# Kernel optimization log

Hardware: AMD Instinct MI355X
Metric: run time of the kernel (lower is better)

The kernel has to match this reference:

```python
import jax, jax.numpy as jnp
import numpy as np

N = 100000
E = 600000
D = 128          # in_channels
D_OUT = 128      # out_channels


def setup_inputs() -> dict:
    key = jax.random.key(0)
    ks = jax.random.split(key, 8)
    node_embeddings = jax.random.normal(ks[0], (N, D), dtype=jnp.float32)
    edge_index = jax.random.randint(ks[1], (2, E), 0, N, dtype=jnp.int64)
    s = 1.0 / np.sqrt(D)
    W_src = jax.random.uniform(ks[2], (D, D), minval=-s, maxval=s, dtype=jnp.float32)
    W_tgt = jax.random.uniform(ks[3], (D, D), minval=-s, maxval=s, dtype=jnp.float32)
    s2 = 1.0 / np.sqrt(2 * D)
    W_proj = jax.random.uniform(ks[4], (2 * D, D_OUT), minval=-s2, maxval=s2, dtype=jnp.float32)
    b_proj = jax.random.uniform(ks[5], (D_OUT,), minval=-s2, maxval=s2, dtype=jnp.float32)
    s3 = 1.0 / np.sqrt(D_OUT)
    W_mlp = jax.random.uniform(ks[6], (D_OUT, D_OUT), minval=-s3, maxval=s3, dtype=jnp.float32)
    b_mlp = jax.random.uniform(ks[7], (D_OUT,), minval=-s3, maxval=s3, dtype=jnp.float32)
    return {
        "node_embeddings": node_embeddings,
        "edge_index": edge_index,
        "W_src": W_src,
        "W_tgt": W_tgt,
        "W_proj": W_proj,
        "b_proj": b_proj,
        "W_mlp": W_mlp,
        "b_mlp": b_mlp,
    }


def reference(node_embeddings, edge_index, W_src, W_tgt, W_proj, b_proj, W_mlp, b_mlp):
    src = node_embeddings[edge_index[0]]   # [E, D]
    tgt = node_embeddings[edge_index[1]]   # [E, D]
    gate_s = jax.nn.sigmoid(src @ W_src)   # Linear no bias + sigmoid
    gate_t = jax.nn.sigmoid(tgt @ W_tgt)
    attn_s = gate_s * src
    attn_t = gate_t * tgt
    edge_attr = jnp.concatenate([attn_s, attn_t], axis=-1)  # [E, 2D]
    edge_attr = edge_attr @ W_proj + b_proj                  # [E, D_OUT]
    return jax.nn.relu(edge_attr) @ W_mlp + b_mlp
```

## Files before the change

### kernel.cpp

```cpp
#include <hip/hip_runtime.h>

#define NN 100000
#define NE 600000
#define DD 128

typedef _Float16 half4_t __attribute__((ext_vector_type(4)));
typedef _Float16 half8_t __attribute__((ext_vector_type(8)));
typedef float f32x4 __attribute__((ext_vector_type(4)));

__device__ __forceinline__ int swzb(int row, int byte) {
  return row * 256 + (byte ^ ((row & 7) << 4));
}

__device__ __forceinline__ half8_t relu_add(half8_t a, half8_t b) {
  half8_t r;
#pragma unroll
  for (int j = 0; j < 8; ++j) {
    const _Float16 s = a[j] + b[j];
    r[j] = s > (_Float16)0 ? s : (_Float16)0;
  }
  return r;
}

__global__ void pack_weights_kernel(const float* __restrict__ Wsrc,
                                    const float* __restrict__ Wtgt,
                                    const float* __restrict__ Wproj,
                                    const float* __restrict__ Wmlp,
                                    _Float16* __restrict__ packed) {
  const int t = (int)blockIdx.x * 256 + (int)threadIdx.x;
  if (t >= 5 * 2048) return;
  const int m = t >> 11;
  const int rem = t & 2047;
  const int nf = rem >> 8;
  const int ks = (rem >> 6) & 3;
  const int l = rem & 63;
  const float* W;
  if (m == 0) W = Wsrc;
  else if (m == 1) W = Wtgt;
  else if (m == 2) W = Wproj;
  else if (m == 3) W = Wproj + 128 * DD;
  else W = Wmlp;
  const int col = (l & 15) + 16 * nf;
  const int k0 = 8 * (l >> 4) + 32 * ks;
  half8_t v;
#pragma unroll
  for (int j = 0; j < 8; ++j) v[j] = (_Float16)W[(size_t)(k0 + j) * DD + col];
  *reinterpret_cast<half8_t*>(packed + (size_t)m * 16384 + (size_t)rem * 8) = v;
}

__global__ void decode_idx_kernel(const unsigned int* __restrict__ eraw,
                                  int* __restrict__ idx) {
  __shared__ int s_is64;
  const int tid = (int)threadIdx.x;
  if (tid < 64) {
    const unsigned long long b = __ballot(eraw[2 * tid + 1] != 0u);
    if (tid == 0) s_is64 = (b == 0ull) ? 1 : 0;
  }
  __syncthreads();
  const int is64 = s_is64;
  const size_t stride = (size_t)gridDim.x * 256;
  for (size_t i = (size_t)blockIdx.x * 256 + tid; i < 2 * (size_t)NE;
       i += stride)
    idx[i] = (int)(is64 ? eraw[2 * i] : eraw[i]);
}

__global__ __launch_bounds__(256, 4)
void phase1_kernel(const float* __restrict__ Xg,
                   const _Float16* __restrict__ packW,
                   const float* __restrict__ bproj,
                   _Float16* __restrict__ Aout,
                   _Float16* __restrict__ Bout) {
  __shared__ _Float16 Xh[64 * DD];
  __shared__ _Float16 Th[64 * DD];
  const int tid = (int)threadIdx.x;
  const int row0 = (int)blockIdx.x * 64;
  const int rem = NN - row0;
  const int nvalid = rem < 64 ? rem : 64;

#pragma unroll
  for (int it = 0; it < 8; ++it) {
    const int i = tid + it * 256;
    const int r = i >> 5;
    const int c4 = i & 31;
    float4 v = make_float4(0.f, 0.f, 0.f, 0.f);
    if (r < nvalid)
      v = reinterpret_cast<const float4*>(Xg + (size_t)(row0 + r) * DD)[c4];
    half4_t h;
    h[0] = (_Float16)v.x; h[1] = (_Float16)v.y;
    h[2] = (_Float16)v.z; h[3] = (_Float16)v.w;
    *reinterpret_cast<half4_t*>(&Xh[swzb(r, c4 * 8) >> 1]) = h;
  }
  __syncthreads();

  const int l = tid & 63;
  const int w = tid >> 6;
  const int lr = l & 15;
  const int lg = l >> 4;

#pragma unroll 1
  for (int p = 0; p < 2; ++p) {
    const _Float16* __restrict__ wb1 = packW + (size_t)p * 16384 + l * 8;
    half8_t w1[2][4];
#pragma unroll
    for (int s = 0; s < 2; ++s)
#pragma unroll
      for (int ks = 0; ks < 4; ++ks)
        w1[s][ks] = *reinterpret_cast<const half8_t*>(
            wb1 + (size_t)(((2 * w + s) * 4 + ks)) * 512);

    f32x4 acc[4][2];
#pragma unroll
    for (int mf = 0; mf < 4; ++mf)
#pragma unroll
      for (int s = 0; s < 2; ++s) acc[mf][s] = (f32x4)0.f;
#pragma unroll
    for (int mf = 0; mf < 4; ++mf) {
      half8_t xf[4];
#pragma unroll
      for (int ks = 0; ks < 4; ++ks)
        xf[ks] = *reinterpret_cast<const half8_t*>(
            &Xh[swzb(mf * 16 + lr, lg * 16 + ks * 64) >> 1]);
#pragma unroll
      for (int ks = 0; ks < 4; ++ks)
#pragma unroll
        for (int s = 0; s < 2; ++s)
          acc[mf][s] = __builtin_amdgcn_mfma_f32_16x16x32_f16(
              w1[s][ks], xf[ks], acc[mf][s], 0, 0, 0);
    }

    if (p) __syncthreads();

#pragma unroll
    for (int mf = 0; mf < 4; ++mf)
#pragma unroll
      for (int s = 0; s < 2; ++s) {
        const int c0 = (2 * w + s) * 16 + lg * 4;
        const int node = mf * 16 + lr;
        const half4_t xh =
            *reinterpret_cast<const half4_t*>(&Xh[swzb(node, c0 * 2) >> 1]);
        half4_t th;
#pragma unroll
        for (int j = 0; j < 4; ++j) {
          const float t = (float)xh[j] / (1.f + __expf(-acc[mf][s][j]));
          th[j] = (_Float16)t;
        }
        *reinterpret_cast<half4_t*>(&Th[swzb(node, c0 * 2) >> 1]) = th;
      }
    __syncthreads();

    const _Float16* __restrict__ wb2 = packW + (size_t)(2 + p) * 16384 + l * 8;
    half8_t w2[2][4];
#pragma unroll
    for (int s = 0; s < 2; ++s)
#pragma unroll
      for (int ks = 0; ks < 4; ++ks)
        w2[s][ks] = *reinterpret_cast<const half8_t*>(
            wb2 + (size_t)(((2 * w + s) * 4 + ks)) * 512);

    f32x4 acc2[4][2];
#pragma unroll
    for (int mf = 0; mf < 4; ++mf)
#pragma unroll
      for (int s = 0; s < 2; ++s) acc2[mf][s] = (f32x4)0.f;
#pragma unroll
    for (int mf = 0; mf < 4; ++mf) {
      half8_t tf[4];
#pragma unroll
      for (int ks = 0; ks < 4; ++ks)
        tf[ks] = *reinterpret_cast<const half8_t*>(
            &Th[swzb(mf * 16 + lr, lg * 16 + ks * 64) >> 1]);
#pragma unroll
      for (int ks = 0; ks < 4; ++ks)
#pragma unroll
        for (int s = 0; s < 2; ++s)
          acc2[mf][s] = __builtin_amdgcn_mfma_f32_16x16x32_f16(
              w2[s][ks], tf[ks], acc2[mf][s], 0, 0, 0);
    }

    _Float16* __restrict__ dst = p ? Bout : Aout;
#pragma unroll
    for (int s = 0; s < 2; ++s) {
      const int c0 = (2 * w + s) * 16 + lg * 4;
      f32x4 bp = (f32x4)0.f;
      if (p == 0) bp = *reinterpret_cast<const f32x4*>(bproj + c0);
#pragma unroll
      for (int mf = 0; mf < 4; ++mf) {
        const int node = mf * 16 + lr;
        if (node < nvalid) {
          const f32x4 v = acc2[mf][s] + bp;
          half4_t h;
#pragma unroll
          for (int j = 0; j < 4; ++j) h[j] = (_Float16)v[j];
          *reinterpret_cast<half4_t*>(dst + (size_t)(row0 + node) * DD + c0) =
              h;
        }
      }
    }
  }
}

__global__ __launch_bounds__(256, 4)
void phase2_kernel(const _Float16* __restrict__ At,
                   const _Float16* __restrict__ Bt,
                   const int* __restrict__ idx,
                   const _Float16* __restrict__ Wpk,
                   const float* __restrict__ bmlp,
                   float* __restrict__ out) {
  __shared__ _Float16 Wl[16384];
  const int tid = (int)threadIdx.x;

#pragma unroll
  for (int i = 0; i < 8; ++i) {
    const int c = tid + i * 256;
    reinterpret_cast<f32x4*>(Wl)[c] =
        reinterpret_cast<const f32x4*>(Wpk)[c];
  }

  const int l = tid & 63;
  const int w = tid >> 6;
  const int lr = l & 15;
  const int lg = l >> 4;
  const int e0 = (int)blockIdx.x * 128 + w * 32;

  const int er0 = e0 + lr;
  const int er1 = e0 + 16 + lr;
  const size_t ec0 = (er0 < NE) ? (size_t)er0 : 0;
  const size_t ec1 = (er1 < NE) ? (size_t)er1 : 0;

  const int ia0 = idx[ec0];
  const int ib0 = idx[(size_t)NE + ec0];
  const int ia1 = idx[ec1];
  const int ib1 = idx[(size_t)NE + ec1];

  const _Float16* __restrict__ pa0 = At + (size_t)ia0 * DD + lg * 8;
  const _Float16* __restrict__ pb0 = Bt + (size_t)ib0 * DD + lg * 8;
  const _Float16* __restrict__ pa1 = At + (size_t)ia1 * DD + lg * 8;
  const _Float16* __restrict__ pb1 = Bt + (size_t)ib1 * DD + lg * 8;

  f32x4 acc[2][8];
#pragma unroll
  for (int mf = 0; mf < 2; ++mf)
#pragma unroll
    for (int nf = 0; nf < 8; ++nf) acc[mf][nf] = (f32x4)0.f;

  half8_t a0 = *reinterpret_cast<const half8_t*>(pa0);
  half8_t b0 = *reinterpret_cast<const half8_t*>(pb0);
  half8_t a1 = *reinterpret_cast<const half8_t*>(pa1);
  half8_t b1 = *reinterpret_cast<const half8_t*>(pb1);

  __syncthreads();

#pragma unroll
  for (int ks = 0; ks < 4; ++ks) {
    half8_t na0, nb0, na1, nb1;
    if (ks < 3) {
      na0 = *reinterpret_cast<const half8_t*>(pa0 + (ks + 1) * 32);
      nb0 = *reinterpret_cast<const half8_t*>(pb0 + (ks + 1) * 32);
      na1 = *reinterpret_cast<const half8_t*>(pa1 + (ks + 1) * 32);
      nb1 = *reinterpret_cast<const half8_t*>(pb1 + (ks + 1) * 32);
    }
    const half8_t r0 = relu_add(a0, b0);
    const half8_t r1 = relu_add(a1, b1);
#pragma unroll
    for (int nf = 0; nf < 8; ++nf) {
      const half8_t wf = *reinterpret_cast<const half8_t*>(
          &Wl[(size_t)(nf * 4 + ks) * 512 + l * 8]);
      acc[0][nf] =
          __builtin_amdgcn_mfma_f32_16x16x32_f16(wf, r0, acc[0][nf], 0, 0, 0);
      acc[1][nf] =
          __builtin_amdgcn_mfma_f32_16x16x32_f16(wf, r1, acc[1][nf], 0, 0, 0);
    }
    if (ks < 3) { a0 = na0; b0 = nb0; a1 = na1; b1 = nb1; }
  }

#pragma unroll
  for (int nf = 0; nf < 8; ++nf) {
    const int c0 = nf * 16 + lg * 4;
    const f32x4 bm = *reinterpret_cast<const f32x4*>(bmlp + c0);
    if (er0 < NE) {
      const f32x4 v = acc[0][nf] + bm;
      __builtin_nontemporal_store(
          v, reinterpret_cast<f32x4*>(out + (size_t)er0 * DD + c0));
    }
    if (er1 < NE) {
      const f32x4 v = acc[1][nf] + bm;
      __builtin_nontemporal_store(
          v, reinterpret_cast<f32x4*>(out + (size_t)er1 * DD + c0));
    }
  }
}

extern "C" void kernel_launch(void* const* d_in, const int* in_sizes, int n_in,
                              void* d_out, int out_size, void* d_ws,
                              size_t ws_size, hipStream_t stream) {
  (void)in_sizes; (void)n_in; (void)out_size; (void)ws_size;

  const float* X = (const float*)d_in[0];
  const unsigned int* eraw = (const unsigned int*)d_in[1];
  const float* Wsrc = (const float*)d_in[2];
  const float* Wtgt = (const float*)d_in[3];
  const float* Wproj = (const float*)d_in[4];
  const float* bproj = (const float*)d_in[5];
  const float* Wmlp = (const float*)d_in[6];
  const float* bmlp = (const float*)d_in[7];
  float* out = (float*)d_out;

  _Float16* A16 = (_Float16*)d_ws;
  _Float16* B16 = A16 + (size_t)NN * DD;
  _Float16* packW = B16 + (size_t)NN * DD;
  int* idx = (int*)(packW + 5 * 16384);

  pack_weights_kernel<<<40, 256, 0, stream>>>(Wsrc, Wtgt, Wproj, Wmlp, packW);
  decode_idx_kernel<<<512, 256, 0, stream>>>(eraw, idx);
  phase1_kernel<<<(NN + 63) / 64, 256, 0, stream>>>(X, packW, bproj, A16, B16);
  phase2_kernel<<<(NE + 127) / 128, 256, 0, stream>>>(A16, B16, idx,
                                                      packW + 4 * 16384, bmlp,
                                                      out);
}
```

Before: 174.7 us.

## Merge prep kernels, shrink phase2 tile to 64 edges and issue gathers first

Merges the weight-packing and index-decoding kernels into one launch to save one kernel launch. Phase2 now handles 16 edges per wave instead of 32, which halves the accumulators, and raises launch bounds from 4 to 5 blocks per CU. All gather loads are issued up front, before the shared-memory weight copy, so their latency overlaps that copy. The costs are twice as many blocks, each reloading the 32KB weight tile into LDS, and less MFMA work per weight fragment read. Bounds checks are dropped, which is safe only because NE divides evenly by 64.

```diff
diff --git a/kernel.cpp b/kernel.cpp
--- a/kernel.cpp
+++ b/kernel.cpp
@@ -22,46 +22,50 @@
   return r;
 }
 
-__global__ void pack_weights_kernel(const float* __restrict__ Wsrc,
-                                    const float* __restrict__ Wtgt,
-                                    const float* __restrict__ Wproj,
-                                    const float* __restrict__ Wmlp,
-                                    _Float16* __restrict__ packed) {
-  const int t = (int)blockIdx.x * 256 + (int)threadIdx.x;
-  if (t >= 5 * 2048) return;
-  const int m = t >> 11;
-  const int rem = t & 2047;
-  const int nf = rem >> 8;
-  const int ks = (rem >> 6) & 3;
-  const int l = rem & 63;
-  const float* W;
-  if (m == 0) W = Wsrc;
-  else if (m == 1) W = Wtgt;
-  else if (m == 2) W = Wproj;
-  else if (m == 3) W = Wproj + 128 * DD;
-  else W = Wmlp;
-  const int col = (l & 15) + 16 * nf;
-  const int k0 = 8 * (l >> 4) + 32 * ks;
-  half8_t v;
-#pragma unroll
-  for (int j = 0; j < 8; ++j) v[j] = (_Float16)W[(size_t)(k0 + j) * DD + col];
-  *reinterpret_cast<half8_t*>(packed + (size_t)m * 16384 + (size_t)rem * 8) = v;
-}
-
-__global__ void decode_idx_kernel(const unsigned int* __restrict__ eraw,
-                                  int* __restrict__ idx) {
-  __shared__ int s_is64;
+__global__ void prep_kernel(const float* __restrict__ Wsrc,
+                            const float* __restrict__ Wtgt,
+                            const float* __restrict__ Wproj,
+                            const float* __restrict__ Wmlp,
+                            const unsigned int* __restrict__ eraw,
+                            int* __restrict__ idx,
+                            _Float16* __restrict__ packed) {
+  const int bid = (int)blockIdx.x;
   const int tid = (int)threadIdx.x;
-  if (tid < 64) {
-    const unsigned long long b = __ballot(eraw[2 * tid + 1] != 0u);
-    if (tid == 0) s_is64 = (b == 0ull) ? 1 : 0;
-  }
-  __syncthreads();
-  const int is64 = s_is64;
-  const size_t stride = (size_t)gridDim.x * 256;
-  for (size_t i = (size_t)blockIdx.x * 256 + tid; i < 2 * (size_t)NE;
-       i += stride)
-    idx[i] = (int)(is64 ? eraw[2 * i] : eraw[i]);
+  if (bid < 40) {
+    const int t = bid * 256 + tid;
+    if (t >= 5 * 2048) return;
+    const int m = t >> 11;
+    const int rem = t & 2047;
+    const int nf = rem >> 8;
+    const int ks = (rem >> 6) & 3;
+    const int l = rem & 63;
+    const float* W;
+    if (m == 0) W = Wsrc;
+    else if (m == 1) W = Wtgt;
+    else if (m == 2) W = Wproj;
+    else if (m == 3) W = Wproj + 128 * DD;
+    else W = Wmlp;
+    const int col = (l & 15) + 16 * nf;
+    const int k0 = 8 * (l >> 4) + 32 * ks;
+    half8_t v;
+#pragma unroll
+    for (int j = 0; j < 8; ++j)
+      v[j] = (_Float16)W[(size_t)(k0 + j) * DD + col];
+    *reinterpret_cast<half8_t*>(packed + (size_t)m * 16384 +
+                                (size_t)rem * 8) = v;
+  } else {
+    __shared__ int s_is64;
+    if (tid < 64) {
+      const unsigned long long b = __ballot(eraw[2 * tid + 1] != 0u);
+      if (tid == 0) s_is64 = (b == 0ull) ? 1 : 0;
+    }
+    __syncthreads();
+    const int is64 = s_is64;
+    const size_t stride = (size_t)512 * 256;
+    for (size_t i = (size_t)(bid - 40) * 256 + tid; i < 2 * (size_t)NE;
+         i += stride)
+      idx[i] = (int)(is64 ? eraw[2 * i] : eraw[i]);
+  }
 }
 
 __global__ __launch_bounds__(256, 4)
@@ -199,7 +203,7 @@
   }
 }
 
-__global__ __launch_bounds__(256, 4)
+__global__ __launch_bounds__(256, 5)
 void phase2_kernel(const _Float16* __restrict__ At,
                    const _Float16* __restrict__ Bt,
                    const int* __restrict__ idx,
@@ -208,85 +212,54 @@
                    float* __restrict__ out) {
   __shared__ _Float16 Wl[16384];
   const int tid = (int)threadIdx.x;
-
-#pragma unroll
-  for (int i = 0; i < 8; ++i) {
-    const int c = tid + i * 256;
-    reinterpret_cast<f32x4*>(Wl)[c] =
-        reinterpret_cast<const f32x4*>(Wpk)[c];
-  }
-
   const int l = tid & 63;
   const int w = tid >> 6;
   const int lr = l & 15;
   const int lg = l >> 4;
-  const int e0 = (int)blockIdx.x * 128 + w * 32;
-
-  const int er0 = e0 + lr;
-  const int er1 = e0 + 16 + lr;
-  const size_t ec0 = (er0 < NE) ? (size_t)er0 : 0;
-  const size_t ec1 = (er1 < NE) ? (size_t)er1 : 0;
-
-  const int ia0 = idx[ec0];
-  const int ib0 = idx[(size_t)NE + ec0];
-  const int ia1 = idx[ec1];
-  const int ib1 = idx[(size_t)NE + ec1];
-
-  const _Float16* __restrict__ pa0 = At + (size_t)ia0 * DD + lg * 8;
-  const _Float16* __restrict__ pb0 = Bt + (size_t)ib0 * DD + lg * 8;
-  const _Float16* __restrict__ pa1 = At + (size_t)ia1 * DD + lg * 8;
-  const _Float16* __restrict__ pb1 = Bt + (size_t)ib1 * DD + lg * 8;
-
-  f32x4 acc[2][8];
-#pragma unroll
-  for (int mf = 0; mf < 2; ++mf)
-#pragma unroll
-    for (int nf = 0; nf < 8; ++nf) acc[mf][nf] = (f32x4)0.f;
-
-  half8_t a0 = *reinterpret_cast<const half8_t*>(pa0);
-  half8_t b0 = *reinterpret_cast<const half8_t*>(pb0);
-  half8_t a1 = *reinterpret_cast<const half8_t*>(pa1);
-  half8_t b1 = *reinterpret_cast<const half8_t*>(pb1);
+  const int er = (int)blockIdx.x * 64 + w * 16 + lr;
+
+  const int ia = idx[er];
+  const int ib = idx[(size_t)NE + er];
+  const _Float16* __restrict__ pa = At + (size_t)ia * DD + lg * 8;
+  const _Float16* __restrict__ pb = Bt + (size_t)ib * DD + lg * 8;
+  half8_t af[4], bf[4];
+#pragma unroll
+  for (int ks = 0; ks < 4; ++ks) {
+    af[ks] = *reinterpret_cast<const half8_t*>(pa + ks * 32);
+    bf[ks] = *reinterpret_cast<const half8_t*>(pb + ks * 32);
+  }
+
+#pragma unroll
+  for (int i = 0; i < 8; ++i) {
+    const int c = tid + i * 256;
+    reinterpret_cast<f32x4*>(Wl)[c] = reinterpret_cast<const f32x4*>(Wpk)[c];
+  }
+
+  f32x4 acc[8];
+#pragma unroll
+  for (int nf = 0; nf < 8; ++nf) acc[nf] = (f32x4)0.f;
 
   __syncthreads();
 
 #pragma unroll
   for (int ks = 0; ks < 4; ++ks) {
-    half8_t na0, nb0, na1, nb1;
-    if (ks < 3) {
-      na0 = *reinterpret_cast<const half8_t*>(pa0 + (ks + 1) * 32);
-      nb0 = *reinterpret_cast<const half8_t*>(pb0 + (ks + 1) * 32);
-      na1 = *reinterpret_cast<const half8_t*>(pa1 + (ks + 1) * 32);
-      nb1 = *reinterpret_cast<const half8_t*>(pb1 + (ks + 1) * 32);
-    }
-    const half8_t r0 = relu_add(a0, b0);
-    const half8_t r1 = relu_add(a1, b1);
+    const half8_t r = relu_add(af[ks], bf[ks]);
 #pragma unroll
     for (int nf = 0; nf < 8; ++nf) {
       const half8_t wf = *reinterpret_cast<const half8_t*>(
           &Wl[(size_t)(nf * 4 + ks) * 512 + l * 8]);
-      acc[0][nf] =
-          __builtin_amdgcn_mfma_f32_16x16x32_f16(wf, r0, acc[0][nf], 0, 0, 0);
-      acc[1][nf] =
-          __builtin_amdgcn_mfma_f32_16x16x32_f16(wf, r1, acc[1][nf], 0, 0, 0);
-    }
-    if (ks < 3) { a0 = na0; b0 = nb0; a1 = na1; b1 = nb1; }
+      acc[nf] =
+          __builtin_amdgcn_mfma_f32_16x16x32_f16(wf, r, acc[nf], 0, 0, 0);
+    }
   }
 
 #pragma unroll
   for (int nf = 0; nf < 8; ++nf) {
     const int c0 = nf * 16 + lg * 4;
     const f32x4 bm = *reinterpret_cast<const f32x4*>(bmlp + c0);
-    if (er0 < NE) {
-      const f32x4 v = acc[0][nf] + bm;
-      __builtin_nontemporal_store(
-          v, reinterpret_cast<f32x4*>(out + (size_t)er0 * DD + c0));
-    }
-    if (er1 < NE) {
-      const f32x4 v = acc[1][nf] + bm;
-      __builtin_nontemporal_store(
-          v, reinterpret_cast<f32x4*>(out + (size_t)er1 * DD + c0));
-    }
+    const f32x4 v = acc[nf] + bm;
+    __builtin_nontemporal_store(
+        v, reinterpret_cast<f32x4*>(out + (size_t)er * DD + c0));
   }
 }
 
@@ -310,10 +283,9 @@
   _Float16* packW = B16 + (size_t)NN * DD;
   int* idx = (int*)(packW + 5 * 16384);
 
-  pack_weights_kernel<<<40, 256, 0, stream>>>(Wsrc, Wtgt, Wproj, Wmlp, packW);
-  decode_idx_kernel<<<512, 256, 0, stream>>>(eraw, idx);
+  prep_kernel<<<552, 256, 0, stream>>>(Wsrc, Wtgt, Wproj, Wmlp, eraw, idx,
+                                       packW);
   phase1_kernel<<<(NN + 63) / 64, 256, 0, stream>>>(X, packW, bproj, A16, B16);
-  phase2_kernel<<<(NE + 127) / 128, 256, 0, stream>>>(A16, B16, idx,
-                                                      packW + 4 * 16384, bmlp,
-                                                      out);
-}
+  phase2_kernel<<<NE / 64, 256, 0, stream>>>(A16, B16, idx,
+                                             packW + 4 * 16384, bmlp, out);
+}
```

After: 173.7 us. No clear change (-0.5%).
